# Kernel optimization log

Hardware: AMD Instinct MI355X
Metric: run time of the kernel (lower is better)

## Reference

```python
import jax, jax.numpy as jnp
import numpy as np
import math

B, S, D, H = 2, 2048, 2048, 16
HD = D // H  # 128
NEG = -1e9


def setup_inputs() -> dict:
    key = jax.random.key(0)
    ks = jax.random.split(key, 6)
    scale = 1.0 / math.sqrt(D)
    x = jax.random.normal(ks[0], (B, S, D), dtype=jnp.float32)
    wq = jax.random.normal(ks[1], (D, D), dtype=jnp.float32) * scale
    wk = jax.random.normal(ks[2], (D, D), dtype=jnp.float32) * scale
    wv = jax.random.normal(ks[3], (D, D), dtype=jnp.float32) * scale
    wo = jax.random.normal(ks[4], (D, D), dtype=jnp.float32) * scale
    # rotary frequencies, standard LLaMA precompute: theta=10000
    inv_freq = 1.0 / (10000.0 ** (jnp.arange(0, HD, 2, dtype=jnp.float32) / HD))  # [HD/2]
    t = jnp.arange(S, dtype=jnp.float32)
    angles = jnp.outer(t, inv_freq)  # [S, HD/2]
    freqs_cos = jnp.cos(angles)
    freqs_sin = jnp.sin(angles)
    # additive causal mask [S, S]
    mask = jnp.where(jnp.triu(jnp.ones((S, S), dtype=bool), k=1), NEG, 0.0).astype(jnp.float32)
    return {"x": x, "wq": wq, "wk": wk, "wv": wv, "wo": wo,
            "freqs_cos": freqs_cos, "freqs_sin": freqs_sin, "mask": mask,
            "start_pos": 0}


def _rope(t, cos, sin):
    # t: [B,S,H,HD]; treat last dim as interleaved (re, im) pairs
    tr = t.reshape(*t.shape[:-1], HD // 2, 2)
    re, im = tr[..., 0], tr[..., 1]
    c = cos[None, :, None, :]  # [1,S,1,HD/2]
    s = sin[None, :, None, :]
    out_re = re * c - im * s
    out_im = re * s + im * c
    return jnp.stack([out_re, out_im], axis=-1).reshape(t.shape)


def reference(x, wq, wk, wv, wo, freqs_cos, freqs_sin, mask, start_pos):
    bsz, seqlen, _ = x.shape
    # torch Linear: y = x @ W^T
    xq = jnp.einsum('bsd,ed->bse', x, wq).reshape(bsz, seqlen, H, HD)
    xk = jnp.einsum('bsd,ed->bse', x, wk).reshape(bsz, seqlen, H, HD)
    xv = jnp.einsum('bsd,ed->bse', x, wv).reshape(bsz, seqlen, H, HD)
    xq = _rope(xq, freqs_cos, freqs_sin)
    xk = _rope(xk, freqs_cos, freqs_sin)
    # scores: [B,H,Sq,Sk]
    scores = jnp.einsum('bqhd,bkhd->bhqk', xq, xk) / math.sqrt(HD)
    scores = scores + mask[None, None, :, :]
    probs = jax.nn.softmax(scores.astype(jnp.float32), axis=-1).astype(xq.dtype)
    out = jnp.einsum('bhqk,bkhd->bqhd', probs, xv).reshape(bsz, seqlen, H * HD)
    return jnp.einsum('bse,de->bsd', out, wo)
```

## Files before the change

kernel.cpp:

```cpp
#include <hip/hip_runtime.h>
#include <cmath>

#define BB 2
#define SS 2048
#define DD 2048
#define HH 16
#define HDD 128
#define MTOT (BB*SS)

typedef float f32x4 __attribute__((ext_vector_type(4)));
typedef short s16x8 __attribute__((ext_vector_type(8)));
typedef short s16x4v __attribute__((ext_vector_type(4)));

static constexpr float NEGV = -1e9f;
static constexpr float SM_SCALE = 0.08838834764831845f;

__device__ __forceinline__ unsigned short f32_to_bf16(float x) {
  unsigned int u = __float_as_uint(x);
  u = u + 0x7FFFu + ((u >> 16) & 1u);
  return (unsigned short)(u >> 16);
}
__device__ __forceinline__ float bf16_to_f32(unsigned short h) {
  return __uint_as_float(((unsigned int)h) << 16);
}
__device__ __forceinline__ void async16(void* ldst, const void* gsrc) {
  __builtin_amdgcn_global_load_lds(
      (const __attribute__((address_space(1))) unsigned int*)gsrc,
      (__attribute__((address_space(3))) unsigned int*)ldst, 16, 0, 0);
}

__global__ __launch_bounds__(256)
void cast_b16(const float* __restrict__ in, unsigned short* __restrict__ out, int n8) {
  int stride = gridDim.x * 256;
  for (int i = blockIdx.x * 256 + threadIdx.x; i < n8; i += stride) {
    const float4* p = (const float4*)in + (size_t)i * 2;
    float4 a = p[0], b = p[1];
    float v[8] = {a.x, a.y, a.z, a.w, b.x, b.y, b.z, b.w};
    s16x8 o;
#pragma unroll
    for (int j = 0; j < 8; ++j) o[j] = (short)f32_to_bf16(v[j]);
    *(s16x8*)(out + (size_t)i * 8) = o;
  }
}

#define GEMM1_BODY                                                             \
  __shared__ unsigned short lds[16 * 512];                                     \
  const int tid = threadIdx.x;                                                 \
  const int l   = tid & 63;                                                    \
  const int w   = tid >> 6;                                                    \
  const int m0  = blockIdx.y * 128;                                            \
  const int n0  = blockIdx.x * 128;                                            \
  const int wm  = w >> 1, wn = w & 1;                                          \
  const unsigned short* mp = (w < 2) ? A : Bm;                                 \
  const int rb = (w < 2) ? m0 : n0;                                            \
  const unsigned short* gs = mp + (size_t)(rb + (w & 1) * 64 + (l & 15)) * K   \
                                + ((l >> 4) * 8);                              \
  unsigned short* ldw = &lds[((w >> 1) * 8 + (w & 1) * 4) * 512];              \
  f32x4 acc[4][4];                                                             \
  _Pragma("unroll") for (int i = 0; i < 4; ++i)                                \
  _Pragma("unroll") for (int j = 0; j < 4; ++j) {                              \
    f32x4 z = {0.f, 0.f, 0.f, 0.f}; acc[i][j] = z; }                           \
  for (int k0 = 0; k0 < K; k0 += 32) {                                         \
    __syncthreads();                                                           \
    _Pragma("unroll") for (int s = 0; s < 4; ++s)                              \
      async16(ldw + s * 512, gs + (size_t)s * 16 * K + k0);                    \
    __syncthreads();                                                           \
    s16x8 ah[4], bh[4];                                                        \
    _Pragma("unroll") for (int i = 0; i < 4; ++i) {                            \
      ah[i] = *(const s16x8*)&lds[(wm * 4 + i) * 512 + l * 8];                 \
      bh[i] = *(const s16x8*)&lds[(8 + wn * 4 + i) * 512 + l * 8];             \
    }                                                                          \
    _Pragma("unroll") for (int i = 0; i < 4; ++i)                              \
    _Pragma("unroll") for (int j = 0; j < 4; ++j)                              \
      acc[i][j] = __builtin_amdgcn_mfma_f32_16x16x32_bf16(ah[i], bh[j], acc[i][j], 0, 0, 0); \
  }                                                                            \
  const int r4 = (l >> 4) * 4, cn = l & 15;

__global__ __launch_bounds__(256)
void gemm_f32(const unsigned short* __restrict__ A, const unsigned short* __restrict__ Bm,
              float* __restrict__ C, int M, int N, int K) {
  GEMM1_BODY
#pragma unroll
  for (int i = 0; i < 4; ++i)
#pragma unroll
    for (int j = 0; j < 4; ++j) {
      float* Cp = C + (size_t)(m0 + wm * 64 + i * 16 + r4) * N + (n0 + wn * 64 + j * 16 + cn);
#pragma unroll
      for (int r = 0; r < 4; ++r) Cp[(size_t)r * N] = acc[i][j][r];
    }
}

__global__ __launch_bounds__(256)
void gemm_b16(const unsigned short* __restrict__ A, const unsigned short* __restrict__ Bm,
              unsigned short* __restrict__ C, int M, int N, int K) {
  GEMM1_BODY
#pragma unroll
  for (int i = 0; i < 4; ++i)
#pragma unroll
    for (int j = 0; j < 4; ++j) {
      size_t idx = (size_t)(m0 + wm * 64 + i * 16 + r4) * N + (n0 + wn * 64 + j * 16 + cn);
#pragma unroll
      for (int r = 0; r < 4; ++r) C[idx + (size_t)r * N] = f32_to_bf16(acc[i][j][r]);
    }
}

__global__ __launch_bounds__(256)
void gemm_b16T(const unsigned short* __restrict__ A, const unsigned short* __restrict__ Bm,
               unsigned short* __restrict__ C, int M, int N, int K) {
  GEMM1_BODY
#pragma unroll
  for (int i = 0; i < 4; ++i)
#pragma unroll
    for (int j = 0; j < 4; ++j) {
      size_t idxT = (size_t)(n0 + wn * 64 + j * 16 + cn) * M + (m0 + wm * 64 + i * 16 + r4);
      s16x4v hv;
#pragma unroll
      for (int r = 0; r < 4; ++r) hv[r] = (short)f32_to_bf16(acc[i][j][r]);
      *(s16x4v*)&C[idxT] = hv;
    }
}

__global__ __launch_bounds__(256)
void rope_b16(unsigned short* __restrict__ Qb, unsigned short* __restrict__ Kb,
              const float* __restrict__ Fc, const float* __restrict__ Fs) {
  int idx = blockIdx.x * 256 + threadIdx.x;
  int m   = idx >> 8;
  int rem = idx & 255;
  int h   = rem >> 4;
  int i4  = rem & 15;
  int s   = m & (SS - 1);
  size_t base = (size_t)m * DD + h * HDD + i4 * 8;
  float4 c  = *(const float4*)&Fc[s * 64 + i4 * 4];
  float4 sn = *(const float4*)&Fs[s * 64 + i4 * 4];
  float cc[4] = {c.x, c.y, c.z, c.w}, ss[4] = {sn.x, sn.y, sn.z, sn.w};
#pragma unroll
  for (int mtx = 0; mtx < 2; ++mtx) {
    unsigned short* Pb = mtx ? Kb : Qb;
    s16x8 v = *(s16x8*)&Pb[base];
    s16x8 o;
#pragma unroll
    for (int p = 0; p < 4; ++p) {
      float re = bf16_to_f32((unsigned short)v[2*p]);
      float im = bf16_to_f32((unsigned short)v[2*p+1]);
      o[2*p]   = (short)f32_to_bf16(re * cc[p] - im * ss[p]);
      o[2*p+1] = (short)f32_to_bf16(re * ss[p] + im * cc[p]);
    }
    *(s16x8*)&Pb[base] = o;
  }
}

#define KB0_ 0
#define VB0_ 8192
#define KB1_ 16384
#define VB1_ 24576
#define PP_  32768

#define STAGE(BUF, KOFF) do {                                                  \
    const int kd_ = (BUF) ? KB1_ : KB0_;                                       \
    const int vd_ = (BUF) ? VB1_ : VB0_;                                       \
    if (w < 2) {                                                               \
      _Pragma("unroll") for (int i_ = 0; i_ < 8; ++i_) {                       \
        int s_ = (w & 1) * 8 + i_;                                             \
        async16(&lds[kd_ + s_ * 512],                                          \
                sb_ + gsl + (size_t)((KOFF) + (s_ >> 2) * 16) * DD + (s_ & 3) * 32); \
      }                                                                        \
    } else {                                                                   \
      _Pragma("unroll") for (int i_ = 0; i_ < 8; ++i_) {                       \
        int s_ = (w & 1) * 8 + i_;                                             \
        async16(&lds[vd_ + s_ * 512],                                          \
                sb_ + gsl + (size_t)(s_ >> 1) * 16 * MTOT + (KOFF) + (s_ & 1) * 32); \
      }                                                                        \
    }                                                                          \
  } while (0)

__global__ __launch_bounds__(256)
void attn_b16(const unsigned short* __restrict__ Qb, const unsigned short* __restrict__ Kb,
              const unsigned short* __restrict__ VTb, unsigned short* __restrict__ Ob) {
  __shared__ unsigned short lds[36864];
  const int tid = threadIdx.x, l = tid & 63, w = tid >> 6;

  const int Dd  = blockIdx.x;
  const int xcd = Dd & 7;
  const int g   = Dd >> 3;
  const int sub = g & 31, ppi = g >> 5;
  const int pair = (xcd << 2) + ppi;
  const int h = pair & 15, b = pair >> 4;
  const int qt = 31 - sub;
  const int q0 = qt * 64;
  const int qrow = q0 + w * 16 + ((l >> 4) << 2);

  const size_t rowQ = (size_t)(b * SS + q0 + w * 16 + (l & 15)) * DD + h * HDD + ((l >> 4) * 8);
  s16x8 qf[4];
#pragma unroll
  for (int t = 0; t < 4; ++t) qf[t] = *(const s16x8*)&Qb[rowQ + t * 32];

  const unsigned short* sb_;
  size_t gsl;
  if (w < 2) { sb_ = Kb;  gsl = (size_t)(b * SS + (l & 15)) * DD + h * HDD + ((l >> 4) * 8); }
  else       { sb_ = VTb; gsl = (size_t)(h * HDD + (l & 15)) * MTOT + b * SS + ((l >> 4) * 8); }

  f32x4 acc[8];
#pragma unroll
  for (int f = 0; f < 8; ++f) { f32x4 z = {0.f,0.f,0.f,0.f}; acc[f] = z; }
  float m_prev[4], l_run[4];
#pragma unroll
  for (int r = 0; r < 4; ++r) { m_prev[r] = -INFINITY; l_run[r] = 0.f; }

  const int nkt = qt + 1;

  STAGE(0, 0);
  __syncthreads();
  int cur = 0;

  for (int t = 0; t < nkt; ++t) {
    const int kb = t * 64;
    if (t + 1 < nkt) STAGE(cur ^ 1, kb + 64);
    const int kbase = cur ? KB1_ : KB0_;
    const int vbase = cur ? VB1_ : VB0_;

    float sc[4][4];
    __builtin_amdgcn_s_setprio(1);
#pragma unroll
    for (int sb = 0; sb < 4; ++sb) {
      f32x4 s = {0.f, 0.f, 0.f, 0.f};
#pragma unroll
      for (int tt = 0; tt < 4; ++tt) {
        s16x8 kf = *(const s16x8*)&lds[kbase + (sb * 4 + tt) * 512 + l * 8];
        s = __builtin_amdgcn_mfma_f32_16x16x32_bf16(qf[tt], kf, s, 0, 0, 0);
      }
      int kcol = kb + sb * 16 + (l & 15);
#pragma unroll
      for (int r = 0; r < 4; ++r)
        sc[sb][r] = (kcol <= qrow + r) ? s[r] * SM_SCALE : NEGV;
    }
    __builtin_amdgcn_s_setprio(0);

    float p[4][4];
#pragma unroll
    for (int r = 0; r < 4; ++r) {
      float tm = fmaxf(fmaxf(sc[0][r], sc[1][r]), fmaxf(sc[2][r], sc[3][r]));
      tm = fmaxf(tm, __shfl_xor(tm, 1));
      tm = fmaxf(tm, __shfl_xor(tm, 2));
      tm = fmaxf(tm, __shfl_xor(tm, 4));
      tm = fmaxf(tm, __shfl_xor(tm, 8));
      float mn = fmaxf(m_prev[r], tm);
      float ps = 0.f;
#pragma unroll
      for (int sb = 0; sb < 4; ++sb) { p[sb][r] = __expf(sc[sb][r] - mn); ps += p[sb][r]; }
      ps += __shfl_xor(ps, 1); ps += __shfl_xor(ps, 2);
      ps += __shfl_xor(ps, 4); ps += __shfl_xor(ps, 8);
      float scl = __expf(m_prev[r] - mn);
      l_run[r] = l_run[r] * scl + ps;
      m_prev[r] = mn;
#pragma unroll
      for (int f = 0; f < 8; ++f) acc[f][r] *= scl;
    }

#pragma unroll
    for (int sb = 0; sb < 4; ++sb)
#pragma unroll
      for (int r = 0; r < 4; ++r) {
        int q   = ((l >> 4) << 2) + r;
        int k32 = ((sb & 1) << 4) + (l & 15);
        int off = ((sb >> 1) << 9) + ((q + ((k32 >> 3) << 4)) << 3) + (k32 & 7);
        lds[PP_ + w * 1024 + off] = f32_to_bf16(p[sb][r]);
      }

    s16x8 pa[2];
#pragma unroll
    for (int ks = 0; ks < 2; ++ks)
      pa[ks] = *(const s16x8*)&lds[PP_ + w * 1024 + ks * 512 + l * 8];
    __builtin_amdgcn_s_setprio(1);
#pragma unroll
    for (int dt = 0; dt < 8; ++dt)
#pragma unroll
      for (int ks = 0; ks < 2; ++ks) {
        s16x8 vf = *(const s16x8*)&lds[vbase + (dt * 2 + ks) * 512 + l * 8];
        acc[dt] = __builtin_amdgcn_mfma_f32_16x16x32_bf16(pa[ks], vf, acc[dt], 0, 0, 0);
      }
    __builtin_amdgcn_s_setprio(0);

    __syncthreads();
    cur ^= 1;
  }

  float rl[4];
#pragma unroll
  for (int r = 0; r < 4; ++r) rl[r] = 1.f / l_run[r];
  const size_t orow = (size_t)(b * SS + q0 + w * 16 + ((l >> 4) << 2)) * DD + h * HDD + (l & 15);
#pragma unroll
  for (int f = 0; f < 8; ++f)
#pragma unroll
    for (int r = 0; r < 4; ++r)
      Ob[orow + (size_t)r * DD + f * 16] = f32_to_bf16(acc[f][r] * rl[r]);
}

extern "C" void kernel_launch(void* const* d_in, const int* in_sizes, int n_in,
                              void* d_out, int out_size, void* d_ws, size_t ws_size,
                              hipStream_t stream) {
  (void)in_sizes; (void)n_in; (void)out_size; (void)ws_size;
  const float* x  = (const float*)d_in[0];
  const float* wq = (const float*)d_in[1];
  const float* wk = (const float*)d_in[2];
  const float* wv = (const float*)d_in[3];
  const float* wo = (const float*)d_in[4];
  const float* fc = (const float*)d_in[5];
  const float* fs = (const float*)d_in[6];
  float* out = (float*)d_out;

  const size_t E = (size_t)MTOT * DD;
  const size_t W = (size_t)DD * DD;

  unsigned short* xb  = (unsigned short*)d_ws;
  unsigned short* Qb  = xb + E;
  unsigned short* Kb  = Qb + E;
  unsigned short* VTb = Kb + E;
  unsigned short* Obf = VTb + E;
  unsigned short* wqb = Obf + E;
  unsigned short* wkb = wqb + W;
  unsigned short* wvb = wkb + W;
  unsigned short* wob = wvb + W;

  dim3 blk(256);
  dim3 gg(DD / 128, MTOT / 128);

  cast_b16<<<dim3(2048), blk, 0, stream>>>(x,  xb,  (int)(E / 8));
  cast_b16<<<dim3(1024), blk, 0, stream>>>(wq, wqb, (int)(W / 8));
  cast_b16<<<dim3(1024), blk, 0, stream>>>(wk, wkb, (int)(W / 8));
  cast_b16<<<dim3(1024), blk, 0, stream>>>(wv, wvb, (int)(W / 8));
  cast_b16<<<dim3(1024), blk, 0, stream>>>(wo, wob, (int)(W / 8));

  gemm_b16 <<<gg, blk, 0, stream>>>(xb, wqb, Qb,  MTOT, DD, DD);
  gemm_b16 <<<gg, blk, 0, stream>>>(xb, wkb, Kb,  MTOT, DD, DD);
  gemm_b16T<<<gg, blk, 0, stream>>>(xb, wvb, VTb, MTOT, DD, DD);

  rope_b16<<<dim3((MTOT * 16 * 16) / 256), blk, 0, stream>>>(Qb, Kb, fc, fs);

  attn_b16<<<dim3(1024), blk, 0, stream>>>(Qb, Kb, VTb, Obf);

  gemm_f32<<<gg, blk, 0, stream>>>(Obf, wob, out, MTOT, DD, DD);
}
```

Before: 574.3 us.

## Double-buffer GEMM LDS loads, fuse QKV projections and weight casts

The GEMM main loop now uses two LDS buffers, so the async global-to-LDS copy for the next K-slice is issued while MFMAs run on the current one, and one barrier per iteration replaces two. The three Q/K/V projection GEMMs are merged into a single launch whose grid covers all three weight matrices, and the four weight casts are merged into one kernel. This removes load-to-compute serialization and several launches, at the cost of doubling LDS use per block, which may lower occupancy.

```diff
diff --git a/kernel.cpp b/kernel.cpp
--- a/kernel.cpp
+++ b/kernel.cpp
@@ -43,80 +43,167 @@
   }
 }
 
-#define GEMM1_BODY                                                             \
-  __shared__ unsigned short lds[16 * 512];                                     \
-  const int tid = threadIdx.x;                                                 \
-  const int l   = tid & 63;                                                    \
-  const int w   = tid >> 6;                                                    \
-  const int m0  = blockIdx.y * 128;                                            \
-  const int n0  = blockIdx.x * 128;                                            \
-  const int wm  = w >> 1, wn = w & 1;                                          \
-  const unsigned short* mp = (w < 2) ? A : Bm;                                 \
-  const int rb = (w < 2) ? m0 : n0;                                            \
-  const unsigned short* gs = mp + (size_t)(rb + (w & 1) * 64 + (l & 15)) * K   \
-                                + ((l >> 4) * 8);                              \
-  unsigned short* ldw = &lds[((w >> 1) * 8 + (w & 1) * 4) * 512];              \
-  f32x4 acc[4][4];                                                             \
-  _Pragma("unroll") for (int i = 0; i < 4; ++i)                                \
-  _Pragma("unroll") for (int j = 0; j < 4; ++j) {                              \
-    f32x4 z = {0.f, 0.f, 0.f, 0.f}; acc[i][j] = z; }                           \
-  for (int k0 = 0; k0 < K; k0 += 32) {                                         \
-    __syncthreads();                                                           \
-    _Pragma("unroll") for (int s = 0; s < 4; ++s)                              \
-      async16(ldw + s * 512, gs + (size_t)s * 16 * K + k0);                    \
-    __syncthreads();                                                           \
-    s16x8 ah[4], bh[4];                                                        \
-    _Pragma("unroll") for (int i = 0; i < 4; ++i) {                            \
-      ah[i] = *(const s16x8*)&lds[(wm * 4 + i) * 512 + l * 8];                 \
-      bh[i] = *(const s16x8*)&lds[(8 + wn * 4 + i) * 512 + l * 8];             \
-    }                                                                          \
-    _Pragma("unroll") for (int i = 0; i < 4; ++i)                              \
-    _Pragma("unroll") for (int j = 0; j < 4; ++j)                              \
-      acc[i][j] = __builtin_amdgcn_mfma_f32_16x16x32_bf16(ah[i], bh[j], acc[i][j], 0, 0, 0); \
-  }                                                                            \
+__global__ __launch_bounds__(256)
+void cast_w4(const float* __restrict__ w0, const float* __restrict__ w1,
+             const float* __restrict__ w2, const float* __restrict__ w3,
+             unsigned short* __restrict__ o0, unsigned short* __restrict__ o1,
+             unsigned short* __restrict__ o2, unsigned short* __restrict__ o3) {
+  const int per = (DD * DD) / 8;
+  int stride = gridDim.x * 256;
+  for (int i = blockIdx.x * 256 + threadIdx.x; i < 4 * per; i += stride) {
+    int which = i >> 19;
+    int off = i & (per - 1);
+    const float* in = (which == 0) ? w0 : (which == 1) ? w1 : (which == 2) ? w2 : w3;
+    unsigned short* out = (which == 0) ? o0 : (which == 1) ? o1 : (which == 2) ? o2 : o3;
+    const float4* p = (const float4*)in + (size_t)off * 2;
+    float4 a = p[0], b = p[1];
+    float v[8] = {a.x, a.y, a.z, a.w, b.x, b.y, b.z, b.w};
+    s16x8 o;
+#pragma unroll
+    for (int j = 0; j < 8; ++j) o[j] = (short)f32_to_bf16(v[j]);
+    *(s16x8*)(out + (size_t)off * 8) = o;
+  }
+}
+
+__global__ __launch_bounds__(256)
+void gemm_qkv(const unsigned short* __restrict__ A,
+              const unsigned short* __restrict__ Wq,
+              const unsigned short* __restrict__ Wk,
+              const unsigned short* __restrict__ Wv,
+              unsigned short* __restrict__ Qb,
+              unsigned short* __restrict__ Kb,
+              unsigned short* __restrict__ VTb) {
+  __shared__ unsigned short lds[32 * 512];
+  const int K = DD;
+  const int tid = threadIdx.x, l = tid & 63, w = tid >> 6;
+  const int m0  = blockIdx.y * 128;
+  const int ng  = blockIdx.x * 128;
+  const int reg = ng >> 11;
+  const int nloc = ng & 2047;
+  const int wm = w >> 1, wn = w & 1;
+  const unsigned short* Bm = (reg == 0) ? Wq : (reg == 1) ? Wk : Wv;
+  const unsigned short* gs = (w < 2)
+      ? A  + (size_t)(m0   + (w & 1) * 64 + (l & 15)) * K + ((l >> 4) * 8)
+      : Bm + (size_t)(nloc + (w & 1) * 64 + (l & 15)) * K + ((l >> 4) * 8);
+  const int ldwoff = ((w >> 1) * 8 + (w & 1) * 4) * 512;
+
+  f32x4 acc[4][4];
+#pragma unroll
+  for (int i = 0; i < 4; ++i)
+#pragma unroll
+    for (int j = 0; j < 4; ++j) { f32x4 z = {0.f,0.f,0.f,0.f}; acc[i][j] = z; }
+
+#pragma unroll
+  for (int s = 0; s < 4; ++s)
+    async16(&lds[ldwoff + s * 512], gs + (size_t)s * 16 * K);
+  __syncthreads();
+  int cur = 0;
+
+  for (int k0 = 0; k0 < K; k0 += 32) {
+    if (k0 + 32 < K) {
+#pragma unroll
+      for (int s = 0; s < 4; ++s)
+        async16(&lds[(cur ^ 1) * 8192 + ldwoff + s * 512],
+                gs + (size_t)s * 16 * K + k0 + 32);
+    }
+    const int base = cur * 8192;
+    s16x8 ah[4], bh[4];
+#pragma unroll
+    for (int i = 0; i < 4; ++i) {
+      ah[i] = *(const s16x8*)&lds[base + (wm * 4 + i) * 512 + l * 8];
+      bh[i] = *(const s16x8*)&lds[base + (8 + wn * 4 + i) * 512 + l * 8];
+    }
+#pragma unroll
+    for (int i = 0; i < 4; ++i)
+#pragma unroll
+      for (int j = 0; j < 4; ++j)
+        acc[i][j] = __builtin_amdgcn_mfma_f32_16x16x32_bf16(ah[i], bh[j], acc[i][j], 0, 0, 0);
+    __syncthreads();
+    cur ^= 1;
+  }
+
   const int r4 = (l >> 4) * 4, cn = l & 15;
-
-__global__ __launch_bounds__(256)
-void gemm_f32(const unsigned short* __restrict__ A, const unsigned short* __restrict__ Bm,
-              float* __restrict__ C, int M, int N, int K) {
-  GEMM1_BODY
+  if (reg < 2) {
+    unsigned short* Cb = (reg == 0) ? Qb : Kb;
+#pragma unroll
+    for (int i = 0; i < 4; ++i)
+#pragma unroll
+      for (int j = 0; j < 4; ++j) {
+        size_t idx = (size_t)(m0 + wm * 64 + i * 16 + r4) * DD + (nloc + wn * 64 + j * 16 + cn);
+#pragma unroll
+        for (int r = 0; r < 4; ++r) Cb[idx + (size_t)r * DD] = f32_to_bf16(acc[i][j][r]);
+      }
+  } else {
+#pragma unroll
+    for (int i = 0; i < 4; ++i)
+#pragma unroll
+      for (int j = 0; j < 4; ++j) {
+        size_t idxT = (size_t)(nloc + wn * 64 + j * 16 + cn) * MTOT + (m0 + wm * 64 + i * 16 + r4);
+        s16x4v hv;
+#pragma unroll
+        for (int r = 0; r < 4; ++r) hv[r] = (short)f32_to_bf16(acc[i][j][r]);
+        *(s16x4v*)&VTb[idxT] = hv;
+      }
+  }
+}
+
+__global__ __launch_bounds__(256)
+void gemm_o(const unsigned short* __restrict__ A, const unsigned short* __restrict__ Bw,
+            float* __restrict__ C) {
+  __shared__ unsigned short lds[32 * 512];
+  const int K = DD;
+  const int tid = threadIdx.x, l = tid & 63, w = tid >> 6;
+  const int m0 = blockIdx.y * 128;
+  const int n0 = blockIdx.x * 128;
+  const int wm = w >> 1, wn = w & 1;
+  const unsigned short* gs = (w < 2)
+      ? A  + (size_t)(m0 + (w & 1) * 64 + (l & 15)) * K + ((l >> 4) * 8)
+      : Bw + (size_t)(n0 + (w & 1) * 64 + (l & 15)) * K + ((l >> 4) * 8);
+  const int ldwoff = ((w >> 1) * 8 + (w & 1) * 4) * 512;
+
+  f32x4 acc[4][4];
 #pragma unroll
   for (int i = 0; i < 4; ++i)
 #pragma unroll
+    for (int j = 0; j < 4; ++j) { f32x4 z = {0.f,0.f,0.f,0.f}; acc[i][j] = z; }
+
+#pragma unroll
+  for (int s = 0; s < 4; ++s)
+    async16(&lds[ldwoff + s * 512], gs + (size_t)s * 16 * K);
+  __syncthreads();
+  int cur = 0;
+
+  for (int k0 = 0; k0 < K; k0 += 32) {
+    if (k0 + 32 < K) {
+#pragma unroll
+      for (int s = 0; s < 4; ++s)
+        async16(&lds[(cur ^ 1) * 8192 + ldwoff + s * 512],
+                gs + (size_t)s * 16 * K + k0 + 32);
+    }
+    const int base = cur * 8192;
+    s16x8 ah[4], bh[4];
+#pragma unroll
+    for (int i = 0; i < 4; ++i) {
+      ah[i] = *(const s16x8*)&lds[base + (wm * 4 + i) * 512 + l * 8];
+      bh[i] = *(const s16x8*)&lds[base + (8 + wn * 4 + i) * 512 + l * 8];
+    }
+#pragma unroll
+    for (int i = 0; i < 4; ++i)
+#pragma unroll
+      for (int j = 0; j < 4; ++j)
+        acc[i][j] = __builtin_amdgcn_mfma_f32_16x16x32_bf16(ah[i], bh[j], acc[i][j], 0, 0, 0);
+    __syncthreads();
+    cur ^= 1;
+  }
+
+  const int r4 = (l >> 4) * 4, cn = l & 15;
+#pragma unroll
+  for (int i = 0; i < 4; ++i)
+#pragma unroll
     for (int j = 0; j < 4; ++j) {
-      float* Cp = C + (size_t)(m0 + wm * 64 + i * 16 + r4) * N + (n0 + wn * 64 + j * 16 + cn);
-#pragma unroll
-      for (int r = 0; r < 4; ++r) Cp[(size_t)r * N] = acc[i][j][r];
-    }
-}
-
-__global__ __launch_bounds__(256)
-void gemm_b16(const unsigned short* __restrict__ A, const unsigned short* __restrict__ Bm,
-              unsigned short* __restrict__ C, int M, int N, int K) {
-  GEMM1_BODY
-#pragma unroll
-  for (int i = 0; i < 4; ++i)
-#pragma unroll
-    for (int j = 0; j < 4; ++j) {
-      size_t idx = (size_t)(m0 + wm * 64 + i * 16 + r4) * N + (n0 + wn * 64 + j * 16 + cn);
-#pragma unroll
-      for (int r = 0; r < 4; ++r) C[idx + (size_t)r * N] = f32_to_bf16(acc[i][j][r]);
-    }
-}
-
-__global__ __launch_bounds__(256)
-void gemm_b16T(const unsigned short* __restrict__ A, const unsigned short* __restrict__ Bm,
-               unsigned short* __restrict__ C, int M, int N, int K) {
-  GEMM1_BODY
-#pragma unroll
-  for (int i = 0; i < 4; ++i)
-#pragma unroll
-    for (int j = 0; j < 4; ++j) {
-      size_t idxT = (size_t)(n0 + wn * 64 + j * 16 + cn) * M + (m0 + wm * 64 + i * 16 + r4);
-      s16x4v hv;
-#pragma unroll
-      for (int r = 0; r < 4; ++r) hv[r] = (short)f32_to_bf16(acc[i][j][r]);
-      *(s16x4v*)&C[idxT] = hv;
+      float* Cp = C + (size_t)(m0 + wm * 64 + i * 16 + r4) * DD + (n0 + wn * 64 + j * 16 + cn);
+#pragma unroll
+      for (int r = 0; r < 4; ++r) Cp[(size_t)r * DD] = acc[i][j][r];
     }
 }
 
@@ -322,21 +409,16 @@
   unsigned short* wob = wvb + W;
 
   dim3 blk(256);
-  dim3 gg(DD / 128, MTOT / 128);
-
-  cast_b16<<<dim3(2048), blk, 0, stream>>>(x,  xb,  (int)(E / 8));
-  cast_b16<<<dim3(1024), blk, 0, stream>>>(wq, wqb, (int)(W / 8));
-  cast_b16<<<dim3(1024), blk, 0, stream>>>(wk, wkb, (int)(W / 8));
-  cast_b16<<<dim3(1024), blk, 0, stream>>>(wv, wvb, (int)(W / 8));
-  cast_b16<<<dim3(1024), blk, 0, stream>>>(wo, wob, (int)(W / 8));
-
-  gemm_b16 <<<gg, blk, 0, stream>>>(xb, wqb, Qb,  MTOT, DD, DD);
-  gemm_b16 <<<gg, blk, 0, stream>>>(xb, wkb, Kb,  MTOT, DD, DD);
-  gemm_b16T<<<gg, blk, 0, stream>>>(xb, wvb, VTb, MTOT, DD, DD);
+
+  cast_b16<<<dim3(2048), blk, 0, stream>>>(x, xb, (int)(E / 8));
+  cast_w4<<<dim3(2048), blk, 0, stream>>>(wq, wk, wv, wo, wqb, wkb, wvb, wob);
+
+  gemm_qkv<<<dim3(3 * DD / 128, MTOT / 128), blk, 0, stream>>>(
+      xb, wqb, wkb, wvb, Qb, Kb, VTb);
 
   rope_b16<<<dim3((MTOT * 16 * 16) / 256), blk, 0, stream>>>(Qb, Kb, fc, fs);
 
   attn_b16<<<dim3(1024), blk, 0, stream>>>(Qb, Kb, VTb, Obf);
 
-  gemm_f32<<<gg, blk, 0, stream>>>(Obf, wob, out, MTOT, DD, DD);
-}
+  gemm_o<<<dim3(DD / 128, MTOT / 128), blk, 0, stream>>>(Obf, wob, out);
+}
```

Measured after the change: 542.4 us. 1.06x faster.
